# Kernel tuning notes

Hardware: AMD Instinct MI355X
Metric: run time of the kernel (lower is better)

## Reference

```python
import jax, jax.numpy as jnp
import numpy as np

N_NODE = 118
DM, DP, DR, DH, DN, DPHI, DE = 768, 128, 128, 256, 256, 192, 256
N_OUT = 2
NEG = -1e9

leaky = lambda z: jnp.where(z >= 0, z, 0.01 * z)


def lstm_layer(x_seq, W_ih, W_hh, b_ih, b_hh):
    # x_seq: [B, T, in]; W_ih: [4H, in]; W_hh: [4H, H]; gate order i,f,g,o (torch)
    B = x_seq.shape[0]
    H = W_hh.shape[1]

    def step(carry, xt):
        h, c = carry
        gates = xt @ W_ih.T + h @ W_hh.T + b_ih + b_hh  # [B, 4H]
        i, f, g, o = jnp.split(gates, 4, axis=1)
        c = jax.nn.sigmoid(f) * c + jax.nn.sigmoid(i) * jnp.tanh(g)
        h = jax.nn.sigmoid(o) * jnp.tanh(c)
        return (h, c), h

    h0 = jnp.zeros((B, H), x_seq.dtype)
    (_, _), hs = jax.lax.scan(step, (h0, h0), jnp.swapaxes(x_seq, 0, 1))
    return jnp.swapaxes(hs, 0, 1)  # [B, T, H]


def setup_inputs() -> dict:
    key = jax.random.key(0)
    ks = jax.random.split(key, 32)
    n_feat, T = 128, 2048
    sc = 0.05
    inp = {}
    inp["x"] = jax.random.normal(ks[0], (N_NODE, T, n_feat), jnp.float32)
    h_pmt = jax.random.uniform(ks[1], (N_NODE, 2), jnp.float32)
    act = jax.random.randint(ks[2], (N_NODE, 1), 0, 2).astype(jnp.float32)
    inp["x_tag"] = jnp.concatenate([h_pmt, act], axis=1)
    # LSTM params (2 layers, hidden=DP)
    inp["W_ih0"] = jax.random.normal(ks[3], (4 * DP, n_feat), jnp.float32) * sc
    inp["W_hh0"] = jax.random.normal(ks[4], (4 * DP, DP), jnp.float32) * sc
    inp["b_ih0"] = jnp.zeros((4 * DP,), jnp.float32)
    inp["b_hh0"] = jnp.zeros((4 * DP,), jnp.float32)
    inp["W_ih1"] = jax.random.normal(ks[5], (4 * DP, DP), jnp.float32) * sc
    inp["W_hh1"] = jax.random.normal(ks[6], (4 * DP, DP), jnp.float32) * sc
    inp["b_ih1"] = jnp.zeros((4 * DP,), jnp.float32)
    inp["b_hh1"] = jnp.zeros((4 * DP,), jnp.float32)
    inp["pseudo_message"] = jax.random.normal(ks[7], (1, DM), jnp.float32) * sc
    inp["Wum"] = jax.random.normal(ks[8], (DM + 1, DR), jnp.float32) * sc
    inp["Wvm"] = jax.random.normal(ks[9], (DM + 1, DR), jnp.float32) * sc
    inp["Wup"] = jax.random.normal(ks[10], (DP, DR), jnp.float32) * sc
    inp["Wvp"] = jax.random.normal(ks[11], (DP, DR), jnp.float32) * sc
    inp["W_hyb"] = jax.random.normal(ks[12], (3 * DR, DH), jnp.float32) * sc
    inp["b_hyb"] = jnp.zeros((DH,), jnp.float32)
    inp["W_act"] = jax.random.normal(ks[13], (DH + 2, DN), jnp.float32) * sc
    inp["b_act"] = jnp.zeros((DN,), jnp.float32)
    inp["W_inact"] = jax.random.normal(ks[14], (DH, DN), jnp.float32) * sc
    inp["b_inact"] = jnp.zeros((DN,), jnp.float32)
    inp["Wphin"] = jax.random.normal(ks[15], (2 * DN, DPHI), jnp.float32) * sc
    inp["aphi"] = jax.random.normal(ks[16], (DPHI, 1), jnp.float32) * sc
    inp["Won"] = jax.random.normal(ks[17], (2 * DN, DN), jnp.float32) * sc
    inp["Weo"] = jax.random.normal(ks[18], (3 * DN, DE), jnp.float32) * sc
    inp["Wi"] = jax.random.normal(ks[19], (N_NODE, DN + 2 * DE, N_OUT), jnp.float32) * sc
    inp["bi"] = jax.random.normal(ks[20], (N_NODE, N_OUT), jnp.float32) * sc
    return inp


def reference(x, x_tag, W_ih0, W_hh0, b_ih0, b_hh0, W_ih1, W_hh1, b_ih1, b_hh1,
              pseudo_message, Wum, Wvm, Wup, Wvp, W_hyb, b_hyb, W_act, b_act,
              W_inact, b_inact, Wphin, aphi, Won, Weo, Wi, bi):
    N = x.shape[0]
    # --- price embedding: 2-layer LSTM, take last hidden ---
    h1 = lstm_layer(x, W_ih0, W_hh0, b_ih0, b_hh0)
    h2 = lstm_layer(h1, W_ih1, W_hh1, b_ih1, b_hh1)
    p = leaky(h2[:, -1, :])  # [N, DP]

    act = x_tag[:, -1:]                      # [N, 1]
    V1 = x_tag[:, -1] == 0
    V0 = x_tag[:, -1] == 1
    m = jnp.broadcast_to(pseudo_message, (N, DM))
    v_m = leaky(jnp.concatenate([m, act], axis=1) @ Wvm)
    u_p = leaky(p @ Wup)
    h_pmt = x_tag[:, 0:2]
    h_hyb = leaky(jnp.concatenate([u_p, u_p + v_m, v_m], axis=1) @ W_hyb + b_hyb)
    n_act = (jnp.concatenate([h_hyb, h_pmt], axis=1) @ W_act + b_act) * (1.0 - act)
    n_inact = (h_hyb @ W_inact + b_inact) * act
    n = leaky(n_act + n_inact)               # [N, DN]

    # pair[i, j] = cat(n[j], n[i])  (matches unsqueeze(0)/unsqueeze(1) repeat order)
    pair = jnp.concatenate([
        jnp.broadcast_to(n[None, :, :], (N, N, DN)),
        jnp.broadcast_to(n[:, None, :], (N, N, DN)),
    ], axis=-1)                               # [N, N, 2*DN]

    phi = (leaky(pair @ Wphin) @ aphi)[..., 0]  # [N, N]
    mask1 = V1[:, None]
    mask0 = V0[:, None]
    phi1 = jax.nn.softmax(jnp.where(mask1, phi, NEG), axis=0)
    phi0 = jax.nn.softmax(jnp.where(mask0, phi, NEG), axis=0)
    phi_masked = jnp.where(mask1, phi1, jnp.where(mask0, phi0, phi))
    phi_all = jax.nn.softmax(phi, axis=0)
    alpha = jnp.where(jnp.sum(V1) > 0, phi_masked, phi_all)

    e = leaky(pair @ Won)
    e = jnp.concatenate([e, pair], axis=-1) @ Weo  # [N, N, DE]
    alpha1 = (1.0 - act) * alpha              # [N, N]
    alpha0 = act * alpha
    hyper_m1 = leaky(jnp.einsum('nj,njd->nd', alpha1, e))
    hyper_m0 = leaky(jnp.einsum('nj,njd->nd', alpha0, e))
    hyper_m = jnp.concatenate([hyper_m0, hyper_m1], axis=-1)
    output = jnp.concatenate([n, hyper_m], axis=-1)  # [N, DN+2*DE]
    y_hat = jnp.einsum('nd,ndo->no', output, Wi) + bi
    y_hat = jax.nn.softmax(y_hat, axis=1)

    o1 = Wum @ Wvm.T
    o2 = Wup @ Wvp.T
    l_ort = jnp.sqrt(jnp.sum(o1 * o1)) + jnp.sqrt(jnp.sum(o2 * o2))

    # vectorized pairwise cosine similarity * sign product over V1 nodes
    nrm = jnp.maximum(jnp.linalg.norm(n, axis=1), 1e-8)
    n_unit = n / nrm[:, None]
    s = jnp.sign(h_pmt[:, 1] - h_pmt[:, 0]) * V1.astype(n.dtype)
    l_pol = jnp.sum((n_unit @ n_unit.T) * (s[:, None] * s[None, :]))

    return (y_hat, h_pmt, l_ort, l_pol, V1, V0)
```

## Files before the change

### kernel.cpp

```cpp
#include <hip/hip_runtime.h>
#include <cstdint>
#include <cstddef>

#define NNODE 118
#define TSEQ  2048
#define TC    256
#define NCH   8
#define TGB   8
#define NEGC  -1000000000.0f

typedef __fp16 f16x8 __attribute__((ext_vector_type(8)));
typedef float floatx4 __attribute__((ext_vector_type(4)));

__device__ __forceinline__ float leakyf(float x){ return x >= 0.f ? x : 0.01f * x; }
__device__ __forceinline__ float frcp(float x){ return __builtin_amdgcn_rcpf(x); }
__device__ __forceinline__ float sigm(float x){ return frcp(1.f + __expf(-x)); }
__device__ __forceinline__ float tanhfast(float x){ return 1.f - 2.f * frcp(__expf(2.f * x) + 1.f); }

__device__ __forceinline__ int swzb(int row, int colByte){
  return row * 256 + (colByte ^ ((row & 7) << 4) ^ ((row & 8) << 2));
}

__device__ float bred_sum(float v, float* buf, int nthr){
  int tid = threadIdx.x;
  buf[tid] = v; __syncthreads();
  for (int s = nthr >> 1; s > 0; s >>= 1){
    if (tid < s) buf[tid] += buf[tid + s];
    __syncthreads();
  }
  float r = buf[0]; __syncthreads(); return r;
}
__device__ float bred_max(float v, float* buf, int nthr){
  int tid = threadIdx.x;
  buf[tid] = v; __syncthreads();
  for (int s = nthr >> 1; s > 0; s >>= 1){
    if (tid < s) buf[tid] = fmaxf(buf[tid], buf[tid + s]);
    __syncthreads();
  }
  float r = buf[0]; __syncthreads(); return r;
}

__global__ void f32_to_f16_k(const float* __restrict__ in, __fp16* __restrict__ out, int n){
  int i = blockIdx.x * blockDim.x + threadIdx.x;
  if (i < n) out[i] = (__fp16)in[i];
}

__global__ __launch_bounds__(256, 2) void gateproj(
    const float* __restrict__ x,
    const __fp16* __restrict__ ringr,
    const __fp16* __restrict__ wiA,
    const __fp16* __restrict__ wiB,
    __fp16* __restrict__ pre1o, __fp16* __restrict__ pre2o,
    int n1blocks, int t0abs)
{
  const int tid = threadIdx.x, lane = tid & 63, w4 = tid >> 6;
  const int q = lane >> 4, l16 = lane & 15;
  const bool isA = (int)blockIdx.x < n1blocks;
  const int bid = isA ? blockIdx.x : (blockIdx.x - n1blocks);
  const int tg = bid >> 3, blk = bid & 7, tbase = tg * TGB;
  const __fp16* Wf = isA ? wiA : wiB;
  __fp16* preo = isA ? pre1o : pre2o;

  __shared__ __fp16 tiles[TGB][2048];

  if (isA){
    const int node = tid >> 4, k8 = tid & 15;
    const int gnode = blk * 16 + node;
    #pragma unroll
    for (int t = 0; t < TGB; t++){
      __fp16 tmp[8];
      if (gnode < NNODE){
        const float* s = x + ((size_t)gnode * TSEQ + (t0abs + tbase + t)) * 128 + k8 * 8;
        float4 a = ((const float4*)s)[0];
        float4 b = ((const float4*)s)[1];
        tmp[0]=(__fp16)a.x; tmp[1]=(__fp16)a.y; tmp[2]=(__fp16)a.z; tmp[3]=(__fp16)a.w;
        tmp[4]=(__fp16)b.x; tmp[5]=(__fp16)b.y; tmp[6]=(__fp16)b.z; tmp[7]=(__fp16)b.w;
      } else {
        #pragma unroll
        for (int i = 0; i < 8; i++) tmp[i] = (__fp16)0.f;
      }
      *(uint4*)((char*)&tiles[t][0] + swzb(node, k8 * 16)) = *(const uint4*)tmp;
    }
  } else {
    #pragma unroll
    for (int t = 0; t < TGB; t++){
      uint4 v = *(const uint4*)((const char*)ringr + (((size_t)(tbase + t) * 8 + blk) * 4096) + tid * 16);
      *(uint4*)((char*)&tiles[t][0] + tid * 16) = v;
    }
  }

  f16x8 WB[2][4][4];
  #pragma unroll
  for (int ws = 0; ws < 2; ws++)
    #pragma unroll
    for (int g = 0; g < 4; g++){
      const int gate = g * 128 + (w4 * 2 + ws) * 16 + l16;
      const __fp16* wp = Wf + (size_t)gate * 128 + q * 8;
      #pragma unroll
      for (int kt = 0; kt < 4; kt++) WB[ws][g][kt] = *(const f16x8*)(wp + kt * 32);
    }
  __syncthreads();

  #pragma unroll 1
  for (int t = 0; t < TGB; t++){
    f16x8 ax[4];
    #pragma unroll
    for (int kt = 0; kt < 4; kt++)
      ax[kt] = *(const f16x8*)((const char*)&tiles[t][0] + swzb(l16, kt * 64 + q * 16));
    #pragma unroll
    for (int ws = 0; ws < 2; ws++)
      #pragma unroll
      for (int g = 0; g < 4; g++){
        floatx4 acc = {0.f, 0.f, 0.f, 0.f};
        #pragma unroll
        for (int kt = 0; kt < 4; kt++)
          acc = __builtin_amdgcn_mfma_f32_16x16x32_f16(ax[kt], WB[ws][g][kt], acc, 0, 0, 0);
        __fp16 o[4];
        o[0]=(__fp16)acc[0]; o[1]=(__fp16)acc[1]; o[2]=(__fp16)acc[2]; o[3]=(__fp16)acc[3];
        const size_t off = (((size_t)(tbase + t) * 8 + blk) * 32 + (size_t)((w4 * 2 + ws) * 4 + g)) * 512;
        *(uint2*)((char*)preo + off + (size_t)lane * 8) = *(const uint2*)o;
      }
  }
}

__global__ __launch_bounds__(512, 2) void lstm_scan(
    const __fp16* __restrict__ pre1, const __fp16* __restrict__ pre2,
    __fp16* __restrict__ ring,
    const __fp16* __restrict__ whh0, const __fp16* __restrict__ whh1,
    const float* __restrict__ b_ih0, const float* __restrict__ b_hh0,
    const float* __restrict__ b_ih1, const float* __restrict__ b_hh1,
    __fp16* __restrict__ hs1, float* __restrict__ c1s,
    __fp16* __restrict__ hs2, float* __restrict__ c2s,
    float* __restrict__ pout, int c)
{
  const bool isL1 = blockIdx.x < 8;
  if (isL1){ if (c >= NCH) return; } else { if (c < 1) return; }
  const int blk = blockIdx.x & 7, n0 = blk * 16;
  const int tid = threadIdx.x, lane = tid & 63, w = tid >> 6;
  const int q = lane >> 4, l16 = lane & 15;

  __shared__ __fp16 hbuf[2][2048];

  const __fp16* prebase = isL1 ? pre1 : pre2;
  const __fp16* Wh = isL1 ? whh0 : whh1;
  const float* bA = isL1 ? b_ih0 : b_ih1;
  const float* bB = isL1 ? b_hh0 : b_hh1;
  __fp16* hst = isL1 ? hs1 : hs2;
  float* cst = isL1 ? c1s : c2s;
  const bool zin = isL1 ? (c == 0) : (c == 1);
  char* ringw = (char*)(ring + (size_t)(c & 1) * TC * 8 * 2048);

  f16x8 WH[4][4];
  float bias[4];
  #pragma unroll
  for (int g = 0; g < 4; g++){
    const int gate = g * 128 + w * 16 + l16;
    const __fp16* wp = Wh + (size_t)gate * 128 + q * 8;
    #pragma unroll
    for (int kt = 0; kt < 4; kt++) WH[g][kt] = *(const f16x8*)(wp + kt * 32);
    bias[g] = bA[gate] + bB[gate];
  }

  float creg[4]; __fp16 hreg[4];
  #pragma unroll
  for (int r = 0; r < 4; r++){
    const int node = q * 4 + r, d = w * 16 + l16;
    __fp16 h0;
    if (zin){ creg[r] = 0.f; h0 = (__fp16)0.f; }
    else { creg[r] = cst[(size_t)(n0 + node) * 128 + d]; h0 = hst[(size_t)(n0 + node) * 128 + d]; }
    hreg[r] = h0;
    *(__fp16*)((char*)&hbuf[1][0] + swzb(node, 2 * d)) = h0;
  }

#define LDPRE(PR, T) do { \
    const char* _b = (const char*)prebase + ((((size_t)(T) * 8 + blk) * 32 + (size_t)(w * 4)) * 512) + (size_t)lane * 8; \
    PR[0] = *(const uint2*)(_b); \
    PR[1] = *(const uint2*)(_b + 512); \
    PR[2] = *(const uint2*)(_b + 1024); \
    PR[3] = *(const uint2*)(_b + 1536); \
  } while (0)

#define STEP(P, CUR, NXT) do { \
    const char* hsrc = (const char*)&hbuf[((P) + 1) & 1][0]; \
    if (isL1 && (P) >= 1){ \
      uint2 hv = *(const uint2*)(hsrc + tid * 8); \
      *(uint2*)(ringw + (((size_t)((P) - 1) * 8 + blk) * 4096) + tid * 8) = hv; \
    } \
    if ((P) + 1 < TC) LDPRE(NXT, (P) + 1); \
    f16x8 ah[4]; \
    _Pragma("unroll") \
    for (int kt = 0; kt < 4; kt++) \
      ah[kt] = *(const f16x8*)(hsrc + swzb(l16, kt * 64 + q * 16)); \
    floatx4 acc[4]; \
    _Pragma("unroll") \
    for (int g = 0; g < 4; g++){ \
      __fp16 pv[4]; \
      *(uint2*)pv = CUR[g]; \
      acc[g][0] = (float)pv[0]; acc[g][1] = (float)pv[1]; \
      acc[g][2] = (float)pv[2]; acc[g][3] = (float)pv[3]; \
    } \
    _Pragma("unroll") \
    for (int kt = 0; kt < 4; kt++){ \
      _Pragma("unroll") \
      for (int g = 0; g < 4; g++) \
        acc[g] = __builtin_amdgcn_mfma_f32_16x16x32_f16(ah[kt], WH[g][kt], acc[g], 0, 0, 0); \
    } \
    char* hdst = (char*)&hbuf[(P) & 1][0]; \
    _Pragma("unroll") \
    for (int r = 0; r < 4; r++){ \
      const float gi = acc[0][r] + bias[0]; \
      const float gf = acc[1][r] + bias[1]; \
      const float gc = acc[2][r] + bias[2]; \
      const float go = acc[3][r] + bias[3]; \
      float cc = sigm(gf) * creg[r] + sigm(gi) * tanhfast(gc); \
      creg[r] = cc; \
      const float h = sigm(go) * tanhfast(cc); \
      hreg[r] = (__fp16)h; \
      *(__fp16*)(hdst + swzb(q * 4 + r, 2 * (w * 16 + l16))) = hreg[r]; \
    } \
    __syncthreads(); \
  } while (0)

  uint2 prA[4], prB[4];
  LDPRE(prA, 0);
  __syncthreads();

  #pragma unroll 1
  for (int p = 0; p < TC; p += 2){
    STEP(p, prA, prB);
    STEP(p + 1, prB, prA);
  }

  if (isL1){
    const char* hsrc = (const char*)&hbuf[(TC - 1) & 1][0];
    uint2 hv = *(const uint2*)(hsrc + tid * 8);
    *(uint2*)(ringw + (((size_t)(TC - 1) * 8 + blk) * 4096) + tid * 8) = hv;
  }
  #pragma unroll
  for (int r = 0; r < 4; r++){
    const int node = q * 4 + r, d = w * 16 + l16;
    const size_t idx = (size_t)(n0 + node) * 128 + d;
    cst[idx] = creg[r];
    hst[idx] = hreg[r];
    if (!isL1 && c == NCH && (n0 + node) < NNODE) pout[idx] = leakyf((float)hreg[r]);
  }
#undef STEP
#undef LDPRE
}

__global__ void node_mlp(
    const float* __restrict__ x_tag, const float* __restrict__ pm,
    const float* __restrict__ Wvm, const float* __restrict__ Wup,
    const float* __restrict__ W_hyb, const float* __restrict__ b_hyb,
    const float* __restrict__ W_act, const float* __restrict__ b_act,
    const float* __restrict__ W_inact, const float* __restrict__ b_inact,
    const float* __restrict__ p, float* __restrict__ nmat)
{
  int n = blockIdx.x, tid = threadIdx.x;
  __shared__ float pl[128], up[128], vm[128], hh[256];
  float act = x_tag[n * 3 + 2], hp0 = x_tag[n * 3 + 0], hp1 = x_tag[n * 3 + 1];
  if (tid < 128) pl[tid] = p[n * 128 + tid];
  __syncthreads();
  if (tid < 128){
    float a1 = 0.f;
    for (int k = 0; k < 768; k++) a1 += pm[k] * Wvm[k * 128 + tid];
    a1 += act * Wvm[768 * 128 + tid];
    vm[tid] = leakyf(a1);
    float a2 = 0.f;
    for (int k = 0; k < 128; k++) a2 += pl[k] * Wup[k * 128 + tid];
    up[tid] = leakyf(a2);
  }
  __syncthreads();
  {
    float a = b_hyb[tid];
    for (int k = 0; k < 128; k++) a += up[k] * W_hyb[k * 256 + tid];
    for (int k = 0; k < 128; k++) a += (up[k] + vm[k]) * W_hyb[(128 + k) * 256 + tid];
    for (int k = 0; k < 128; k++) a += vm[k] * W_hyb[(256 + k) * 256 + tid];
    hh[tid] = leakyf(a);
  }
  __syncthreads();
  {
    float na = b_act[tid];
    for (int k = 0; k < 256; k++) na += hh[k] * W_act[k * 256 + tid];
    na += hp0 * W_act[256 * 256 + tid] + hp1 * W_act[257 * 256 + tid];
    float ni = b_inact[tid];
    for (int k = 0; k < 256; k++) ni += hh[k] * W_inact[k * 256 + tid];
    nmat[n * 256 + tid] = leakyf(na * (1.f - act) + ni * act);
  }
}

__global__ void node_proj(
    const float* __restrict__ nmat,
    const float* __restrict__ Wphin, const float* __restrict__ Won,
    const float* __restrict__ Weo,
    float* __restrict__ A, float* __restrict__ B,
    float* __restrict__ C, float* __restrict__ D,
    float* __restrict__ Q, float* __restrict__ R)
{
  int n = blockIdx.x, tid = threadIdx.x;
  __shared__ float nl[256];
  nl[tid] = nmat[n * 256 + tid];
  __syncthreads();
  if (tid < 192){
    float a = 0.f, b = 0.f;
    for (int k = 0; k < 256; k++){ float v = nl[k]; a += v * Wphin[k * 192 + tid]; b += v * Wphin[(256 + k) * 192 + tid]; }
    A[n * 192 + tid] = a; B[n * 192 + tid] = b;
  }
  float c = 0.f, d = 0.f, q = 0.f, r = 0.f;
  for (int k = 0; k < 256; k++){
    float v = nl[k];
    c += v * Won[k * 256 + tid];
    d += v * Won[(256 + k) * 256 + tid];
    q += v * Weo[(256 + k) * 256 + tid];
    r += v * Weo[(512 + k) * 256 + tid];
  }
  C[n * 256 + tid] = c; D[n * 256 + tid] = d;
  Q[n * 256 + tid] = q; R[n * 256 + tid] = r;
}

__global__ void phi_kernel(const float* __restrict__ A, const float* __restrict__ B,
                           const float* __restrict__ aphi, float* __restrict__ phiT)
{
  int j = blockIdx.x, tid = threadIdx.x;
  __shared__ float Aj[192], ap[192];
  for (int k = tid; k < 192; k += 128){ Aj[k] = A[j * 192 + k]; ap[k] = aphi[k]; }
  __syncthreads();
  if (tid < NNODE){
    const float* Bi = B + (size_t)tid * 192;
    float s = 0.f;
    for (int k = 0; k < 192; k++) s += leakyf(Aj[k] + Bi[k]) * ap[k];
    phiT[j * NNODE + tid] = s;
  }
}

__global__ void alpha_kernel(const float* __restrict__ phiT, const float* __restrict__ x_tag,
                             float* __restrict__ alpha)
{
  int j = blockIdx.x, tid = threadIdx.x;
  __shared__ float buf[128];
  bool valid = tid < NNODE;
  float ph = valid ? phiT[j * NNODE + tid] : 0.f;
  float a  = valid ? x_tag[tid * 3 + 2] : -1.f;
  bool v1 = (a == 0.f), v0 = (a == 1.f);

  float c1 = bred_sum((valid && v1) ? 1.f : 0.f, buf, 128);

  float x1 = (valid && v1) ? ph : NEGC;
  float m1 = bred_max(valid ? x1 : -3.4e38f, buf, 128);
  float e1 = valid ? __expf(x1 - m1) : 0.f;
  float s1 = bred_sum(e1, buf, 128);
  float p1 = e1 / s1;

  float x0 = (valid && v0) ? ph : NEGC;
  float m0 = bred_max(valid ? x0 : -3.4e38f, buf, 128);
  float e0 = valid ? __expf(x0 - m0) : 0.f;
  float s0 = bred_sum(e0, buf, 128);
  float p0 = e0 / s0;

  float ma = bred_max(valid ? ph : -3.4e38f, buf, 128);
  float ea = valid ? __expf(ph - ma) : 0.f;
  float sa = bred_sum(ea, buf, 128);
  float pa = ea / sa;

  float pmask = v1 ? p1 : (v0 ? p0 : ph);
  float al = (c1 > 0.f) ? pmask : pa;
  if (valid) alpha[tid * NNODE + j] = al;
}

__global__ void att_sum(const float* __restrict__ alpha, const float* __restrict__ C,
                        const float* __restrict__ D, const float* __restrict__ Q,
                        const float* __restrict__ R, const float* __restrict__ nmat,
                        float* __restrict__ T1, float* __restrict__ Spart,
                        float* __restrict__ nrm)
{
  int i = blockIdx.x, tid = threadIdx.x;
  __shared__ float al[128];
  __shared__ float rb[256];
  if (tid < 128) al[tid] = (tid < NNODE) ? alpha[i * NNODE + tid] : 0.f;
  __syncthreads();
  float Di = D[i * 256 + tid];
  float acc1 = 0.f, acc2 = 0.f, sa = 0.f;
  for (int jj = 0; jj < NNODE; jj++){
    float av = al[jj]; sa += av;
    acc1 += av * leakyf(C[jj * 256 + tid] + Di);
    acc2 += av * Q[jj * 256 + tid];
  }
  T1[i * 256 + tid] = acc1;
  Spart[i * 256 + tid] = acc2 + sa * R[i * 256 + tid];
  float nv = nmat[i * 256 + tid];
  float ss = bred_sum(nv * nv, rb, 256);
  if (tid == 0) nrm[i] = fmaxf(sqrtf(ss), 1e-8f);
}

__global__ void finalize_node(const float* __restrict__ T1, const float* __restrict__ Spart,
                              const float* __restrict__ Weo, const float* __restrict__ nmat,
                              const float* __restrict__ x_tag, const float* __restrict__ Wi,
                              const float* __restrict__ bi, const float* __restrict__ nrm,
                              float* __restrict__ vvec, float* __restrict__ out)
{
  int i = blockIdx.x, tid = threadIdx.x;
  __shared__ float t1[256];
  __shared__ float rb[256];
  t1[tid] = T1[i * 256 + tid];
  __syncthreads();
  float s = Spart[i * 256 + tid];
  for (int k = 0; k < 256; k++) s += t1[k] * Weo[k * 256 + tid];
  float act = x_tag[i * 3 + 2], hp0 = x_tag[i * 3 + 0], hp1 = x_tag[i * 3 + 1];
  float hm0 = leakyf(act * s);
  float hm1 = leakyf((1.f - act) * s);
  float nd = nmat[i * 256 + tid];
  const float* Wir = Wi + (size_t)i * 1536;
  float y0 = nd * Wir[tid * 2]     + hm0 * Wir[(256 + tid) * 2]     + hm1 * Wir[(512 + tid) * 2];
  float y1 = nd * Wir[tid * 2 + 1] + hm0 * Wir[(256 + tid) * 2 + 1] + hm1 * Wir[(512 + tid) * 2 + 1];
  y0 = bred_sum(y0, rb, 256);
  y1 = bred_sum(y1, rb, 256);
  float sgn = (hp1 > hp0) ? 1.f : ((hp1 < hp0) ? -1.f : 0.f);
  if (act == 0.f && sgn != 0.f) atomicAdd(vvec + tid, sgn * nd / nrm[i]);
  if (tid == 0){
    y0 += bi[i * 2]; y1 += bi[i * 2 + 1];
    float m = fmaxf(y0, y1);
    float ee0 = __expf(y0 - m), ee1 = __expf(y1 - m);
    float ssum = ee0 + ee1;
    out[i * 2]     = ee0 / ssum;
    out[i * 2 + 1] = ee1 / ssum;
    out[236 + i * 2]     = hp0;
    out[236 + i * 2 + 1] = hp1;
    out[474 + i] = (act == 0.f) ? 1.f : 0.f;
    out[592 + i] = (act == 1.f) ? 1.f : 0.f;
  }
}

__global__ void ort_kernel(const float* __restrict__ Wum, const float* __restrict__ Wvm,
                           const float* __restrict__ Wup, const float* __restrict__ Wvp,
                           float* __restrict__ misc)
{
  int a = blockIdx.x, b = threadIdx.x;
  float g1 = 0.f, g2 = 0.f, g3 = 0.f, g4 = 0.f;
  for (int r = 0; r < 769; r++){
    g1 += Wum[r * 128 + a] * Wum[r * 128 + b];
    g2 += Wvm[r * 128 + a] * Wvm[r * 128 + b];
  }
  for (int r = 0; r < 128; r++){
    g3 += Wup[r * 128 + a] * Wup[r * 128 + b];
    g4 += Wvp[r * 128 + a] * Wvp[r * 128 + b];
  }
  __shared__ float rb[128];
  float s1 = bred_sum(g1 * g2, rb, 128);
  float s2 = bred_sum(g3 * g4, rb, 128);
  if (b == 0){ atomicAdd(misc + 0, s1); atomicAdd(misc + 1, s2); }
}

__global__ void finalize_scalars(const float* __restrict__ misc, const float* __restrict__ vvec,
                                 float* __restrict__ out)
{
  __shared__ float rb[256];
  int tid = threadIdx.x;
  float v = vvec[tid];
  float ss = bred_sum(v * v, rb, 256);
  if (tid == 0){
    out[472] = sqrtf(misc[0]) + sqrtf(misc[1]);
    out[473] = ss;
  }
}

extern "C" void kernel_launch(void* const* d_in, const int* in_sizes, int n_in,
                              void* d_out, int out_size, void* d_ws, size_t ws_size,
                              hipStream_t stream)
{
  const float* x        = (const float*)d_in[0];
  const float* x_tag    = (const float*)d_in[1];
  const float* W_ih0    = (const float*)d_in[2];
  const float* W_hh0    = (const float*)d_in[3];
  const float* b_ih0    = (const float*)d_in[4];
  const float* b_hh0    = (const float*)d_in[5];
  const float* W_ih1    = (const float*)d_in[6];
  const float* W_hh1    = (const float*)d_in[7];
  const float* b_ih1    = (const float*)d_in[8];
  const float* b_hh1    = (const float*)d_in[9];
  const float* pm       = (const float*)d_in[10];
  const float* Wum      = (const float*)d_in[11];
  const float* Wvm      = (const float*)d_in[12];
  const float* Wup      = (const float*)d_in[13];
  const float* Wvp      = (const float*)d_in[14];
  const float* W_hyb    = (const float*)d_in[15];
  const float* b_hyb    = (const float*)d_in[16];
  const float* W_act    = (const float*)d_in[17];
  const float* b_act    = (const float*)d_in[18];
  const float* W_inact  = (const float*)d_in[19];
  const float* b_inact  = (const float*)d_in[20];
  const float* Wphin    = (const float*)d_in[21];
  const float* aphi     = (const float*)d_in[22];
  const float* Won      = (const float*)d_in[23];
  const float* Weo      = (const float*)d_in[24];
  const float* Wi       = (const float*)d_in[25];
  const float* bi       = (const float*)d_in[26];
  float* out = (float*)d_out;

  char* base = (char*)d_ws;
  size_t off = 0;
  auto take = [&](size_t bytes) -> char* {
    char* p = base + off;
    off += (bytes + 255) & ~(size_t)255;
    return p;
  };
  __fp16* pre1   = (__fp16*)take((size_t)TC * 8 * 32 * 512);
  __fp16* pre2   = (__fp16*)take((size_t)TC * 8 * 32 * 512);
  __fp16* h1ring = (__fp16*)take((size_t)2 * TC * 8 * 2048 * 2);
  __fp16* wih0h  = (__fp16*)take((size_t)512 * 128 * 2);
  __fp16* wih1h  = (__fp16*)take((size_t)512 * 128 * 2);
  __fp16* whh0h  = (__fp16*)take((size_t)512 * 128 * 2);
  __fp16* whh1h  = (__fp16*)take((size_t)512 * 128 * 2);
  __fp16* hs1    = (__fp16*)take((size_t)128 * 128 * 2);
  float* c1s     = (float*)take((size_t)128 * 128 * 4);
  __fp16* hs2    = (__fp16*)take((size_t)128 * 128 * 2);
  float* c2s     = (float*)take((size_t)128 * 128 * 4);
  float* pbuf  = (float*)take((size_t)NNODE * 128 * 4);
  float* nmat  = (float*)take((size_t)NNODE * 256 * 4);
  float* Amat  = (float*)take((size_t)NNODE * 192 * 4);
  float* Bmat  = (float*)take((size_t)NNODE * 192 * 4);
  float* Cmat  = (float*)take((size_t)NNODE * 256 * 4);
  float* Dmat  = (float*)take((size_t)NNODE * 256 * 4);
  float* Qmat  = (float*)take((size_t)NNODE * 256 * 4);
  float* Rmat  = (float*)take((size_t)NNODE * 256 * 4);
  float* phiT  = (float*)take((size_t)NNODE * NNODE * 4);
  float* alpha = (float*)take((size_t)NNODE * NNODE * 4);
  float* T1    = (float*)take((size_t)NNODE * 256 * 4);
  float* Spart = (float*)take((size_t)NNODE * 256 * 4);
  float* nrm   = (float*)take((size_t)NNODE * 4);
  float* vvec  = (float*)take(256 * 4);
  float* misc  = (float*)take(8 * 4);

  hipMemsetAsync(vvec, 0, 1024 + 32, stream);

  f32_to_f16_k<<<256, 256, 0, stream>>>(W_ih0, wih0h, 512 * 128);
  f32_to_f16_k<<<256, 256, 0, stream>>>(W_ih1, wih1h, 512 * 128);
  f32_to_f16_k<<<256, 256, 0, stream>>>(W_hh0, whh0h, 512 * 128);
  f32_to_f16_k<<<256, 256, 0, stream>>>(W_hh1, whh1h, 512 * 128);

  const size_t ringslot = (size_t)TC * 8 * 2048;
  const int gpb = (TC / TGB) * 8;
  for (int c = 0; c <= NCH; c++){
    const int n1 = (c < NCH) ? gpb : 0;
    const int n2 = (c >= 1) ? gpb : 0;
    if (n1 + n2 > 0)
      gateproj<<<n1 + n2, 256, 0, stream>>>(x, h1ring + (size_t)((c - 1) & 1) * ringslot,
                                            wih0h, wih1h, pre1, pre2, n1, c * TC);
    lstm_scan<<<16, 512, 0, stream>>>(pre1, pre2, h1ring, whh0h, whh1h,
                                      b_ih0, b_hh0, b_ih1, b_hh1,
                                      hs1, c1s, hs2, c2s, pbuf, c);
  }

  node_mlp<<<NNODE, 256, 0, stream>>>(x_tag, pm, Wvm, Wup, W_hyb, b_hyb,
                                      W_act, b_act, W_inact, b_inact, pbuf, nmat);
  node_proj<<<NNODE, 256, 0, stream>>>(nmat, Wphin, Won, Weo, Amat, Bmat, Cmat, Dmat, Qmat, Rmat);
  phi_kernel<<<NNODE, 128, 0, stream>>>(Amat, Bmat, aphi, phiT);
  alpha_kernel<<<NNODE, 128, 0, stream>>>(phiT, x_tag, alpha);
  att_sum<<<NNODE, 256, 0, stream>>>(alpha, Cmat, Dmat, Qmat, Rmat, nmat, T1, Spart, nrm);
  finalize_node<<<NNODE, 256, 0, stream>>>(T1, Spart, Weo, nmat, x_tag, Wi, bi, nrm, vvec, out);
  ort_kernel<<<128, 128, 0, stream>>>(Wum, Wvm, Wup, Wvp, misc);
  finalize_scalars<<<1, 256, 0, stream>>>(misc, vvec, out);
}
```

Before: 3.293 ms.

## Batch LSTM h ring writes every 8 steps and vectorize pre-activation loads

Measured after the change: 3.350 ms. About the same (+1.7%).

```diff
diff --git a/kernel.cpp b/kernel.cpp
--- a/kernel.cpp
+++ b/kernel.cpp
@@ -108,7 +108,8 @@
     for (int kt = 0; kt < 4; kt++)
       ax[kt] = *(const f16x8*)((const char*)&tiles[t][0] + swzb(l16, kt * 64 + q * 16));
     #pragma unroll
-    for (int ws = 0; ws < 2; ws++)
+    for (int ws = 0; ws < 2; ws++){
+      const size_t off = ((((size_t)(tbase + t) * 8 + blk) * 8 + (size_t)(w4 * 2 + ws)) * 64 + (size_t)lane) * 32;
       #pragma unroll
       for (int g = 0; g < 4; g++){
         floatx4 acc = {0.f, 0.f, 0.f, 0.f};
@@ -117,9 +118,9 @@
           acc = __builtin_amdgcn_mfma_f32_16x16x32_f16(ax[kt], WB[ws][g][kt], acc, 0, 0, 0);
         __fp16 o[4];
         o[0]=(__fp16)acc[0]; o[1]=(__fp16)acc[1]; o[2]=(__fp16)acc[2]; o[3]=(__fp16)acc[3];
-        const size_t off = (((size_t)(tbase + t) * 8 + blk) * 32 + (size_t)((w4 * 2 + ws) * 4 + g)) * 512;
-        *(uint2*)((char*)preo + off + (size_t)lane * 8) = *(const uint2*)o;
+        *(uint2*)((char*)preo + off + g * 8) = *(const uint2*)o;
       }
+    }
   }
 }
 
@@ -139,7 +140,7 @@
   const int tid = threadIdx.x, lane = tid & 63, w = tid >> 6;
   const int q = lane >> 4, l16 = lane & 15;
 
-  __shared__ __fp16 hbuf[2][2048];
+  __shared__ __fp16 hhist[16][2048];
 
   const __fp16* prebase = isL1 ? pre1 : pre2;
   const __fp16* Wh = isL1 ? whh0 : whh1;
@@ -169,43 +170,47 @@
     if (zin){ creg[r] = 0.f; h0 = (__fp16)0.f; }
     else { creg[r] = cst[(size_t)(n0 + node) * 128 + d]; h0 = hst[(size_t)(n0 + node) * 128 + d]; }
     hreg[r] = h0;
-    *(__fp16*)((char*)&hbuf[1][0] + swzb(node, 2 * d)) = h0;
+    *(__fp16*)((char*)&hhist[15][0] + swzb(node, 2 * d)) = h0;
   }
 
 #define LDPRE(PR, T) do { \
-    const char* _b = (const char*)prebase + ((((size_t)(T) * 8 + blk) * 32 + (size_t)(w * 4)) * 512) + (size_t)lane * 8; \
-    PR[0] = *(const uint2*)(_b); \
-    PR[1] = *(const uint2*)(_b + 512); \
-    PR[2] = *(const uint2*)(_b + 1024); \
-    PR[3] = *(const uint2*)(_b + 1536); \
+    const char* _b = (const char*)prebase + ((((size_t)(T) * 8 + blk) * 8 + (size_t)w) * 64 + (size_t)lane) * 32; \
+    PR[0] = ((const uint4*)_b)[0]; \
+    PR[1] = ((const uint4*)_b)[1]; \
   } while (0)
 
 #define STEP(P, CUR, NXT) do { \
-    const char* hsrc = (const char*)&hbuf[((P) + 1) & 1][0]; \
-    if (isL1 && (P) >= 1){ \
-      uint2 hv = *(const uint2*)(hsrc + tid * 8); \
-      *(uint2*)(ringw + (((size_t)((P) - 1) * 8 + blk) * 4096) + tid * 8) = hv; \
+    const char* hsrc = (const char*)&hhist[((P) + 15) & 15][0]; \
+    if (isL1 && (P) >= 8 && (((P) & 7) == 0)){ \
+      const int half_ = ((P) & 8) ? 0 : 8;       \
+      _Pragma("unroll") \
+      for (int s_ = 0; s_ < 8; s_++){ \
+        uint2 hv = *(const uint2*)((const char*)&hhist[half_ + s_][0] + tid * 8); \
+        *(uint2*)(ringw + (((size_t)((P) - 8 + s_) * 8 + blk) * 4096) + tid * 8) = hv; \
+      } \
+    } \
+    floatx4 acc[4]; \
+    { \
+      __fp16 pva[8], pvb[8]; \
+      *(uint4*)pva = CUR[0]; *(uint4*)pvb = CUR[1]; \
+      _Pragma("unroll") \
+      for (int i_ = 0; i_ < 4; i_++){ \
+        acc[0][i_] = (float)pva[i_];     acc[1][i_] = (float)pva[4 + i_]; \
+        acc[2][i_] = (float)pvb[i_];     acc[3][i_] = (float)pvb[4 + i_]; \
+      } \
     } \
     if ((P) + 1 < TC) LDPRE(NXT, (P) + 1); \
     f16x8 ah[4]; \
     _Pragma("unroll") \
     for (int kt = 0; kt < 4; kt++) \
       ah[kt] = *(const f16x8*)(hsrc + swzb(l16, kt * 64 + q * 16)); \
-    floatx4 acc[4]; \
-    _Pragma("unroll") \
-    for (int g = 0; g < 4; g++){ \
-      __fp16 pv[4]; \
-      *(uint2*)pv = CUR[g]; \
-      acc[g][0] = (float)pv[0]; acc[g][1] = (float)pv[1]; \
-      acc[g][2] = (float)pv[2]; acc[g][3] = (float)pv[3]; \
-    } \
     _Pragma("unroll") \
     for (int kt = 0; kt < 4; kt++){ \
       _Pragma("unroll") \
       for (int g = 0; g < 4; g++) \
         acc[g] = __builtin_amdgcn_mfma_f32_16x16x32_f16(ah[kt], WH[g][kt], acc[g], 0, 0, 0); \
     } \
-    char* hdst = (char*)&hbuf[(P) & 1][0]; \
+    char* hdst = (char*)&hhist[(P) & 15][0]; \
     _Pragma("unroll") \
     for (int r = 0; r < 4; r++){ \
       const float gi = acc[0][r] + bias[0]; \
@@ -221,7 +226,7 @@
     __syncthreads(); \
   } while (0)
 
-  uint2 prA[4], prB[4];
+  uint4 prA[2], prB[2];
   LDPRE(prA, 0);
   __syncthreads();
 
@@ -232,9 +237,11 @@
   }
 
   if (isL1){
-    const char* hsrc = (const char*)&hbuf[(TC - 1) & 1][0];
-    uint2 hv = *(const uint2*)(hsrc + tid * 8);
-    *(uint2*)(ringw + (((size_t)(TC - 1) * 8 + blk) * 4096) + tid * 8) = hv;
+    #pragma unroll
+    for (int s_ = 0; s_ < 8; s_++){
+      uint2 hv = *(const uint2*)((const char*)&hhist[8 + s_][0] + tid * 8);
+      *(uint2*)(ringw + (((size_t)(TC - 8 + s_) * 8 + blk) * 4096) + tid * 8) = hv;
+    }
   }
   #pragma unroll
   for (int r = 0; r < 4; r++){
```
